# Kernel optimization log

Hardware: AMD Instinct MI355X
Metric: run time of the kernel (lower is better)

## Reference

```python
import jax, jax.numpy as jnp
import numpy as np

HIDDEN = 1024
HEADS = 16
HEAD_DIM = HIDDEN // HEADS
ROPE_THETA = 10000.0
WINDOW = 128
NEG_INF = -1e9


def _rope_cos_sin(seq_len, head_dim, theta, dtype):
    # inv_freq: [dh/2]; emb = concat([freqs, freqs]) to match rotate-half convention
    inv_freq = 1.0 / (theta ** (jnp.arange(0, head_dim, 2, dtype=jnp.float32) / head_dim))
    pos = jnp.arange(seq_len, dtype=jnp.float32)
    freqs = jnp.einsum('s,d->sd', pos, inv_freq)          # [S, dh/2]
    emb = jnp.concatenate([freqs, freqs], axis=-1)        # [S, dh]
    return jnp.cos(emb).astype(dtype), jnp.sin(emb).astype(dtype)


def _apply_rope(x, cos, sin):
    # x: [B, S, H, dh]; cos/sin: [S, dh] broadcast over batch and heads
    x1, x2 = jnp.split(x, 2, axis=-1)
    half_rot = jnp.concatenate([-x2, x1], axis=-1)
    c = cos[None, :, None, :]
    s = sin[None, :, None, :]
    return x * c + half_rot * s


def setup_inputs() -> dict:
    key = jax.random.key(0)
    k1, k2, k3, k4, k5 = jax.random.split(key, 5)
    std = 0.02
    return {
        'hidden_states': jax.random.normal(k1, (2, 2048, HIDDEN), dtype=jnp.float32),
        'Wq': jax.random.normal(k2, (HIDDEN, HEADS, HEAD_DIM), dtype=jnp.float32) * std,
        'Wk': jax.random.normal(k3, (HIDDEN, HEADS, HEAD_DIM), dtype=jnp.float32) * std,
        'Wv': jax.random.normal(k4, (HIDDEN, HEADS, HEAD_DIM), dtype=jnp.float32) * std,
        'Wo': jax.random.normal(k5, (HEADS, HEAD_DIM, HIDDEN), dtype=jnp.float32) * std,
    }


def reference(hidden_states, Wq, Wk, Wv, Wo):
    B, S, D = hidden_states.shape
    x4 = hidden_states.reshape(B, S, HEADS, HEAD_DIM)
    cos, sin = _rope_cos_sin(S, HEAD_DIM, ROPE_THETA, hidden_states.dtype)
    # RoPE applied to raw hidden states (pre-projection), per original module
    q_in = _apply_rope(x4, cos, sin).reshape(B, S, D)
    k_in = q_in  # query and key get identical RoPE of the same tensor
    v_in = hidden_states

    q = jnp.einsum('bsd,dhk->bshk', q_in, Wq)  # [B,S,H,dh]
    k = jnp.einsum('bsd,dhk->bshk', k_in, Wk)
    v = jnp.einsum('bsd,dhk->bshk', v_in, Wv)

    scale = 1.0 / jnp.sqrt(jnp.asarray(HEAD_DIM, dtype=q.dtype))
    scores = jnp.einsum('bqhd,bkhd->bhqk', q, k) * scale  # [B,H,S,S]

    # sliding-window mask: |i - j| < WINDOW
    pos = jnp.arange(S)
    win = jnp.abs(pos[:, None] - pos[None, :]) < WINDOW   # [S,S] bool
    scores = jnp.where(win[None, None, :, :], scores, NEG_INF)

    probs = jax.nn.softmax(scores, axis=-1)
    out = jnp.einsum('bhqk,bkhd->bqhd', probs, v)          # [B,S,H,dh]
    return jnp.einsum('bqhd,hdo->bqo', out, Wo)            # [B,S,D]
```

## Files before the change

### kernel.cpp

```cpp
#include <hip/hip_runtime.h>
#include <hip/hip_bf16.h>
#include <cstdint>
#include <cmath>

typedef __bf16 bf16_t;
typedef __bf16 bf16x8 __attribute__((ext_vector_type(8)));
typedef __bf16 bf16x4 __attribute__((ext_vector_type(4)));
typedef float  f32x4  __attribute__((ext_vector_type(4)));

#define MFMA16(a, b, c) __builtin_amdgcn_mfma_f32_16x16x32_bf16(a, b, c, 0, 0, 0)

constexpr int   SS    = 2048;
constexpr int   DD    = 1024;
constexpr int   HH    = 16;
constexpr float SCALE = 0.125f;
constexpr float L2E   = 1.44269504088896f;

__device__ __forceinline__ bool detect_fp32(const uint16_t* w) {
    uint16_t v = w[threadIdx.x & 63];
    int e = (v >> 7) & 0xFF;
    unsigned long long m = __ballot(e >= 0x80);
    return __popcll(m) >= 4;
}

__device__ __forceinline__ float ldin(const void* p, size_t i, bool f32) {
    return f32 ? ((const float*)p)[i] : (float)((const bf16_t*)p)[i];
}

__device__ __forceinline__ void gload_lds16(const bf16_t* g, bf16_t* l) {
    __builtin_amdgcn_global_load_lds(
        (const __attribute__((address_space(1))) void*)(g),
        (__attribute__((address_space(3))) void*)(l), 16, 0, 0);
}

__global__ __launch_bounds__(256) void prep_kernel(
    const void* __restrict__ hidden, const void* __restrict__ Wq,
    const void* __restrict__ Wk, const void* __restrict__ Wv,
    const void* __restrict__ Wo,
    bf16_t* __restrict__ roped, bf16_t* __restrict__ hiddenb,
    bf16_t* __restrict__ WqT, bf16_t* __restrict__ WkT,
    bf16_t* __restrict__ WvT, bf16_t* __restrict__ WoT) {
    const bool f32 = detect_fp32((const uint16_t*)Wq);
    __shared__ bf16_t tile[32][33];
    if (blockIdx.x < 1024) {
        int gid = blockIdx.x * 256 + threadIdx.x;
        int ic = (gid & 3) * 8;
        int h  = (gid >> 2) & 15;
        int s  = (gid >> 6) & 2047;
        int b  = gid >> 17;
        size_t base = ((size_t)(b * SS + s)) * DD + h * 64 + ic;
        float x[8], y[8];
        if (f32) {
            const float* hp = (const float*)hidden;
            f32x4 x0 = *(const f32x4*)(hp + base);
            f32x4 x1 = *(const f32x4*)(hp + base + 4);
            f32x4 y0 = *(const f32x4*)(hp + base + 32);
            f32x4 y1 = *(const f32x4*)(hp + base + 36);
#pragma unroll
            for (int j = 0; j < 4; ++j) {
                x[j] = x0[j]; x[4 + j] = x1[j];
                y[j] = y0[j]; y[4 + j] = y1[j];
            }
        } else {
            const bf16_t* hp = (const bf16_t*)hidden;
            bf16x8 xv = *(const bf16x8*)(hp + base);
            bf16x8 yv = *(const bf16x8*)(hp + base + 32);
#pragma unroll
            for (int j = 0; j < 8; ++j) { x[j] = (float)xv[j]; y[j] = (float)yv[j]; }
        }
        bf16x8 ro, rh;
#pragma unroll
        for (int j = 0; j < 8; ++j) {
            int i = ic + j;
            float invf = exp2f(-(float)i * (13.287712379549449f / 32.0f));
            float sn, cs;
            __sincosf((float)s * invf, &sn, &cs);
            ro[j]  = (bf16_t)(x[j] * cs - y[j] * sn);
            rh[j]  = (bf16_t)(y[j] * cs + x[j] * sn);
        }
        *(bf16x8*)(roped + base)      = ro;
        *(bf16x8*)(roped + base + 32) = rh;
        if (f32) {
            bf16x8 hb0, hb1;
#pragma unroll
            for (int j = 0; j < 8; ++j) { hb0[j] = (bf16_t)x[j]; hb1[j] = (bf16_t)y[j]; }
            *(bf16x8*)(hiddenb + base)      = hb0;
            *(bf16x8*)(hiddenb + base + 32) = hb1;
        }
    } else {
        int w = blockIdx.x - 1024;
        int z = w >> 10;
        int yy = (w >> 5) & 31, xx = w & 31;
        const void* src = (z == 0) ? Wq : (z == 1) ? Wk : (z == 2) ? Wv : Wo;
        bf16_t*     dst = (z == 0) ? WqT : (z == 1) ? WkT : (z == 2) ? WvT : WoT;
        int tx = threadIdx.x & 31, ty = threadIdx.x >> 5;
        int x0 = xx * 32, y0 = yy * 32;
#pragma unroll
        for (int j = 0; j < 4; ++j)
            tile[ty + j * 8][tx] =
                (bf16_t)ldin(src, (size_t)(y0 + ty + j * 8) * DD + x0 + tx, f32);
        __syncthreads();
#pragma unroll
        for (int j = 0; j < 4; ++j)
            dst[(size_t)(x0 + ty + j * 8) * DD + y0 + tx] = tile[tx][ty + j * 8];
    }
}

__device__ __forceinline__ void stage_a128(const bf16_t* A, int m0, int k0,
                                           bf16_t* As, int tid) {
#pragma unroll
    for (int i = 0; i < 4; ++i) {
        int c = tid + i * 256;
        int r = c >> 3, g = (c & 7) ^ (r & 7);
        gload_lds16(A + (size_t)(m0 + r) * DD + k0 + g * 8, As + c * 8);
    }
}
__device__ __forceinline__ void stage_b64(const bf16_t* Bt, int n0, int k0,
                                          bf16_t* Bs, int tid) {
#pragma unroll
    for (int i = 0; i < 2; ++i) {
        int c = tid + i * 256;
        int r = c >> 3, g = (c & 7) ^ (r & 7);
        gload_lds16(Bt + (size_t)(n0 + r) * DD + k0 + g * 8, Bs + c * 8);
    }
}

__global__ __launch_bounds__(256, 3) void gemm_qkv(
    const bf16_t* __restrict__ roped, const void* __restrict__ hidden_raw,
    const bf16_t* __restrict__ hiddenb, const uint16_t* __restrict__ wdet,
    const bf16_t* __restrict__ WqT, const bf16_t* __restrict__ WkT,
    const bf16_t* __restrict__ WvT,
    bf16_t* __restrict__ Qo, bf16_t* __restrict__ Ko, bf16_t* __restrict__ Vt) {
    __shared__ __align__(16) bf16_t As[128 * 64];
    __shared__ __align__(16) bf16_t Bs[128 * 64];
    const int tid = threadIdx.x, lane = tid & 63, quad = lane >> 4, l16 = lane & 15;
    const int wave = tid >> 6, wm = (wave >> 1) * 64, wn = (wave & 1) * 64;
    const int sw = l16 & 7;

    const int lin = blockIdx.x;
    const int xcd = lin & 7;
    const int t8  = lin >> 3;
    const int z   = t8 >> 5;
    const int mb  = t8 & 31;
    const int m0  = mb * 128, n0 = xcd * 128;

    const bf16_t* A;
    const bf16_t* B;
    if (z == 0)      { A = roped; B = WqT; }
    else if (z == 1) { A = roped; B = WkT; }
    else {
        const bool f32 = detect_fp32(wdet);
        A = f32 ? hiddenb : (const bf16_t*)hidden_raw;
        B = WvT;
    }

    f32x4 acc[4][4];
#pragma unroll
    for (int i = 0; i < 4; ++i)
#pragma unroll
        for (int j = 0; j < 4; ++j) acc[i][j] = (f32x4)0.0f;

    for (int k0 = 0; k0 < DD; k0 += 64) {
        stage_a128(A, m0, k0, As, tid);
        stage_a128(B, n0, k0, Bs, tid);
        __syncthreads();
#pragma unroll
        for (int half = 0; half < 2; ++half) {
            const int h4 = half * 4;
            bf16x8 af[4], bf[4];
#pragma unroll
            for (int t = 0; t < 4; ++t) {
                af[t] = *(const bf16x8*)(As + (wm + t * 16 + l16) * 64 + ((h4 + quad) ^ sw) * 8);
                bf[t] = *(const bf16x8*)(Bs + (wn + t * 16 + l16) * 64 + ((h4 + quad) ^ sw) * 8);
            }
#pragma unroll
            for (int i = 0; i < 4; ++i)
#pragma unroll
                for (int j = 0; j < 4; ++j)
                    acc[i][j] = MFMA16(af[i], bf[j], acc[i][j]);
        }
        __syncthreads();
    }

    if (z < 2) {
        bf16_t* O = (z == 0) ? Qo : Ko;
#pragma unroll
        for (int i = 0; i < 4; ++i) {
            int mbase = m0 + wm + i * 16 + quad * 4;
            int b = mbase >> 11, sl = mbase & 2047;
#pragma unroll
            for (int j = 0; j < 4; ++j) {
                int n = n0 + wn + j * 16 + l16;
                int h = n >> 6, d = n & 63;
                size_t base = (((size_t)b * HH + h) * SS + sl) * 64 + d;
#pragma unroll
                for (int r = 0; r < 4; ++r)
                    O[base + 64 * r] = (bf16_t)acc[i][j][r];
            }
        }
    } else {
#pragma unroll
        for (int i = 0; i < 4; ++i) {
            int mbase = m0 + wm + i * 16 + quad * 4;
            int b = mbase >> 11, sl = mbase & 2047;
#pragma unroll
            for (int j = 0; j < 4; ++j) {
                int n = n0 + wn + j * 16 + l16;
                int h = n >> 6, d = n & 63;
                bf16x4 v;
                v[0] = (bf16_t)acc[i][j][0]; v[1] = (bf16_t)acc[i][j][1];
                v[2] = (bf16_t)acc[i][j][2]; v[3] = (bf16_t)acc[i][j][3];
                *(bf16x4*)(Vt + (((size_t)b * HH + h) * 64 + d) * SS + sl) = v;
            }
        }
    }
}

__global__ __launch_bounds__(256) void attn_kernel(
    const bf16_t* __restrict__ Q, const bf16_t* __restrict__ Kk,
    const bf16_t* __restrict__ Vt, bf16_t* __restrict__ attn) {
    __shared__ __align__(16) bf16_t Ks[2][32 * 64];
    __shared__ __align__(16) bf16_t Vs[2][64 * 32];
    __shared__ __align__(16) bf16_t Pl[4][16 * 40];
    const int tid = threadIdx.x, wave = tid >> 6, lane = tid & 63;
    const int quad = lane >> 4, l16 = lane & 15;
    const int sw7 = l16 & 7, sw3 = l16 & 3;

    int lin = (blockIdx.x >> 3) + 128 * (blockIdx.x & 7);
    const int qb0 = (lin & 31) * 64;
    const int h   = (lin >> 5) & 15;
    const int b   = lin >> 9;
    const int qw  = qb0 + wave * 16;

    const size_t bh = (size_t)b * HH + h;
    const bf16_t* Qp = Q  + bh * SS * 64;
    const bf16_t* Kp = Kk + bh * SS * 64;
    const bf16_t* Vp = Vt + bh * 64 * SS;
    bf16_t* P = &Pl[wave][0];

    bf16x8 q0 = *(const bf16x8*)(Qp + (size_t)(qw + l16) * 64 + quad * 8);
    bf16x8 q1 = *(const bf16x8*)(Qp + (size_t)(qw + l16) * 64 + 32 + quad * 8);

    f32x4 Oacc[4];
#pragma unroll
    for (int t = 0; t < 4; ++t) Oacc[t] = (f32x4)0.0f;
    float lsum[4] = {0.f, 0.f, 0.f, 0.f};

    int lo = qb0 - 127; if (lo < 0) lo = 0; lo &= ~31;
    int hi = qb0 + 63 + 127; if (hi > SS - 1) hi = SS - 1;

    const int krow = tid >> 3, kcol = ((tid & 7) ^ (krow & 7)) * 8;
    const int vrow = tid >> 2, vcol = ((tid & 3) ^ (vrow & 3)) * 8;

    int parity = 0;
    for (int kt = lo; kt <= hi; kt += 32, parity ^= 1) {
        gload_lds16(Kp + (size_t)(kt + krow) * 64 + kcol, &Ks[parity][0] + tid * 8);
        gload_lds16(Vp + (size_t)vrow * SS + kt + vcol, &Vs[parity][0] + tid * 8);
        __syncthreads();

        const bf16_t* Kl = &Ks[parity][0];
        const bf16_t* Vl = &Vs[parity][0];
        bf16x8 k00 = *(const bf16x8*)(Kl + l16 * 64 + (quad ^ sw7) * 8);
        bf16x8 k01 = *(const bf16x8*)(Kl + l16 * 64 + ((quad + 4) ^ sw7) * 8);
        bf16x8 k10 = *(const bf16x8*)(Kl + (16 + l16) * 64 + (quad ^ sw7) * 8);
        bf16x8 k11 = *(const bf16x8*)(Kl + (16 + l16) * 64 + ((quad + 4) ^ sw7) * 8);
        bf16x8 vf[4];
#pragma unroll
        for (int t = 0; t < 4; ++t)
            vf[t] = *(const bf16x8*)(Vl + (t * 16 + l16) * 32 + (quad ^ sw3) * 8);

        __builtin_amdgcn_s_setprio(1);
        f32x4 s0 = MFMA16(q0, k00, (f32x4)0.0f);  s0 = MFMA16(q1, k01, s0);
        f32x4 s1 = MFMA16(q0, k10, (f32x4)0.0f);  s1 = MFMA16(q1, k11, s1);
        __builtin_amdgcn_s_setprio(0);

        const int kr0 = kt + l16, kr1 = kt + 16 + l16;
#pragma unroll
        for (int r = 0; r < 4; ++r) {
            int qa = qw + quad * 4 + r;
            int d0 = qa - kr0; if (d0 < 0) d0 = -d0;
            int d1 = qa - kr1; if (d1 < 0) d1 = -d1;
            float p0 = (d0 < 128) ? exp2f(s0[r] * (SCALE * L2E)) : 0.0f;
            float p1 = (d1 < 128) ? exp2f(s1[r] * (SCALE * L2E)) : 0.0f;
            lsum[r] += p0 + p1;
            P[(quad * 4 + r) * 40 + l16]      = (bf16_t)p0;
            P[(quad * 4 + r) * 40 + 16 + l16] = (bf16_t)p1;
        }
        __asm__ volatile("s_waitcnt lgkmcnt(0)" ::: "memory");
        bf16x8 pf = *(const bf16x8*)(P + l16 * 40 + quad * 8);
        __builtin_amdgcn_s_setprio(1);
#pragma unroll
        for (int t = 0; t < 4; ++t)
            Oacc[t] = MFMA16(pf, vf[t], Oacc[t]);
        __builtin_amdgcn_s_setprio(0);
    }

#pragma unroll
    for (int r = 0; r < 4; ++r) {
        float l = lsum[r];
        l += __shfl_xor(l, 1, 64);
        l += __shfl_xor(l, 2, 64);
        l += __shfl_xor(l, 4, 64);
        l += __shfl_xor(l, 8, 64);
        float inv = 1.0f / l;
        int sa = qw + quad * 4 + r;
        size_t base = (((size_t)b * SS + sa) * HH + h) * 64 + l16;
        attn[base]      = (bf16_t)(Oacc[0][r] * inv);
        attn[base + 16] = (bf16_t)(Oacc[1][r] * inv);
        attn[base + 32] = (bf16_t)(Oacc[2][r] * inv);
        attn[base + 48] = (bf16_t)(Oacc[3][r] * inv);
    }
}

__global__ __launch_bounds__(256, 4) void gemm_out_kernel(
    const bf16_t* __restrict__ A, const bf16_t* __restrict__ WoT,
    const uint16_t* __restrict__ wdet, void* __restrict__ out) {
    __shared__ __align__(16) bf16_t As[128 * 64];
    __shared__ __align__(16) bf16_t B1[64 * 64];
    const int tid = threadIdx.x, lane = tid & 63, quad = lane >> 4, l16 = lane & 15;
    const int wave = tid >> 6, wm = (wave >> 1) * 64, wn = (wave & 1) * 32;
    const int sw = l16 & 7;

    const int lin = blockIdx.x;
    const int xcd = lin & 7, s = lin >> 3;
    const int mb = (xcd >> 1) * 8 + (s >> 3);
    const int nb = (xcd & 1) * 8 + (s & 7);
    const int m0 = mb * 128, n0 = nb * 64;

    f32x4 acc[4][2];
#pragma unroll
    for (int i = 0; i < 4; ++i)
#pragma unroll
        for (int j = 0; j < 2; ++j) acc[i][j] = (f32x4)0.0f;

    for (int k0 = 0; k0 < DD; k0 += 64) {
        stage_a128(A, m0, k0, As, tid);
        stage_b64(WoT, n0, k0, B1, tid);
        __syncthreads();
#pragma unroll
        for (int half = 0; half < 2; ++half) {
            const int h4 = half * 4;
            bf16x8 af[4], b1f[2];
#pragma unroll
            for (int t = 0; t < 4; ++t)
                af[t] = *(const bf16x8*)(As + (wm + t * 16 + l16) * 64 + ((h4 + quad) ^ sw) * 8);
#pragma unroll
            for (int t = 0; t < 2; ++t)
                b1f[t] = *(const bf16x8*)(B1 + (wn + t * 16 + l16) * 64 + ((h4 + quad) ^ sw) * 8);
#pragma unroll
            for (int i = 0; i < 4; ++i)
#pragma unroll
                for (int j = 0; j < 2; ++j)
                    acc[i][j] = MFMA16(af[i], b1f[j], acc[i][j]);
        }
        __syncthreads();
    }

    const bool f32 = detect_fp32(wdet);
#pragma unroll
    for (int i = 0; i < 4; ++i) {
        int mbase = m0 + wm + i * 16 + quad * 4;
#pragma unroll
        for (int j = 0; j < 2; ++j) {
            int n = n0 + wn + j * 16 + l16;
#pragma unroll
            for (int r = 0; r < 4; ++r) {
                size_t idx = (size_t)(mbase + r) * DD + n;
                if (f32) ((float*)out)[idx] = acc[i][j][r];
                else     ((bf16_t*)out)[idx] = (bf16_t)acc[i][j][r];
            }
        }
    }
}

extern "C" void kernel_launch(void* const* d_in, const int* in_sizes, int n_in,
                              void* d_out, int out_size, void* d_ws, size_t ws_size,
                              hipStream_t stream) {
    const void* hidden = d_in[0];
    const void* Wq = d_in[1];
    const void* Wk = d_in[2];
    const void* Wv = d_in[3];
    const void* Wo = d_in[4];
    const uint16_t* wdet = (const uint16_t*)d_in[1];
    char* ws = (char*)d_ws;

    bf16_t* roped   = (bf16_t*)(ws);
    bf16_t* hiddenb = (bf16_t*)(ws + ( 8u << 20));
    bf16_t* WqT     = (bf16_t*)(ws + (16u << 20));
    bf16_t* WkT     = (bf16_t*)(ws + (18u << 20));
    bf16_t* WvT     = (bf16_t*)(ws + (20u << 20));
    bf16_t* WoT     = (bf16_t*)(ws + (22u << 20));
    bf16_t* Qb      = (bf16_t*)(ws + (24u << 20));
    bf16_t* Kb      = (bf16_t*)(ws + (32u << 20));
    bf16_t* Vt      = (bf16_t*)(ws + (40u << 20));
    bf16_t* attn    = roped;

    hipLaunchKernelGGL(prep_kernel, dim3(5120), dim3(256), 0, stream,
                       hidden, Wq, Wk, Wv, Wo, roped, hiddenb,
                       WqT, WkT, WvT, WoT);
    hipLaunchKernelGGL(gemm_qkv, dim3(768), dim3(256), 0, stream,
                       roped, hidden, hiddenb, wdet, WqT, WkT, WvT, Qb, Kb, Vt);
    hipLaunchKernelGGL(attn_kernel, dim3(1024), dim3(256), 0, stream,
                       Qb, Kb, Vt, attn);
    hipLaunchKernelGGL(gemm_out_kernel, dim3(512), dim3(256), 0, stream,
                       attn, WoT, wdet, d_out);
}
```

Baseline: 157.8 us.

## Use 32x32 MFMA in GEMMs and widen attention tiles to 128 queries

Both GEMM kernels switch from 16x16x32 to 32x32x16 bf16 MFMA with 16-wide accumulators, which changes the fragment loads and the epilogue index mapping. The goal is fewer LDS reads per MFMA. The attention kernel now uses 512-thread blocks covering 128 queries, with 64-key K/V tiles. Half the threads load K and half load V, so each block issues fewer barriers and loads per key. The trade-off is higher register and LDS pressure, and attention runs with half as many blocks.

```diff
diff --git a/kernel.cpp b/kernel.cpp
--- a/kernel.cpp
+++ b/kernel.cpp
@@ -7,8 +7,10 @@
 typedef __bf16 bf16x8 __attribute__((ext_vector_type(8)));
 typedef __bf16 bf16x4 __attribute__((ext_vector_type(4)));
 typedef float  f32x4  __attribute__((ext_vector_type(4)));
+typedef float  f32x16 __attribute__((ext_vector_type(16)));
 
 #define MFMA16(a, b, c) __builtin_amdgcn_mfma_f32_16x16x32_bf16(a, b, c, 0, 0, 0)
+#define MFMA32(a, b, c) __builtin_amdgcn_mfma_f32_32x32x16_bf16(a, b, c, 0, 0, 0)
 
 constexpr int   SS    = 2048;
 constexpr int   DD    = 1024;
@@ -133,9 +135,10 @@
     bf16_t* __restrict__ Qo, bf16_t* __restrict__ Ko, bf16_t* __restrict__ Vt) {
     __shared__ __align__(16) bf16_t As[128 * 64];
     __shared__ __align__(16) bf16_t Bs[128 * 64];
-    const int tid = threadIdx.x, lane = tid & 63, quad = lane >> 4, l16 = lane & 15;
+    const int tid = threadIdx.x, lane = tid & 63;
+    const int l32 = lane & 31, kh = lane >> 5;
     const int wave = tid >> 6, wm = (wave >> 1) * 64, wn = (wave & 1) * 64;
-    const int sw = l16 & 7;
+    const int sw = l32 & 7;
 
     const int lin = blockIdx.x;
     const int xcd = lin & 7;
@@ -154,30 +157,27 @@
         B = WvT;
     }
 
-    f32x4 acc[4][4];
-#pragma unroll
-    for (int i = 0; i < 4; ++i)
-#pragma unroll
-        for (int j = 0; j < 4; ++j) acc[i][j] = (f32x4)0.0f;
+    f32x16 acc[2][2];
+#pragma unroll
+    for (int i = 0; i < 2; ++i)
+#pragma unroll
+        for (int j = 0; j < 2; ++j) acc[i][j] = (f32x16)0.0f;
 
     for (int k0 = 0; k0 < DD; k0 += 64) {
         stage_a128(A, m0, k0, As, tid);
         stage_a128(B, n0, k0, Bs, tid);
         __syncthreads();
 #pragma unroll
-        for (int half = 0; half < 2; ++half) {
-            const int h4 = half * 4;
-            bf16x8 af[4], bf[4];
-#pragma unroll
-            for (int t = 0; t < 4; ++t) {
-                af[t] = *(const bf16x8*)(As + (wm + t * 16 + l16) * 64 + ((h4 + quad) ^ sw) * 8);
-                bf[t] = *(const bf16x8*)(Bs + (wn + t * 16 + l16) * 64 + ((h4 + quad) ^ sw) * 8);
-            }
-#pragma unroll
-            for (int i = 0; i < 4; ++i)
-#pragma unroll
-                for (int j = 0; j < 4; ++j)
-                    acc[i][j] = MFMA16(af[i], bf[j], acc[i][j]);
+        for (int kk = 0; kk < 4; ++kk) {
+            const int c8 = (kk * 2 + kh) ^ sw;
+            bf16x8 a0 = *(const bf16x8*)(As + (wm      + l32) * 64 + c8 * 8);
+            bf16x8 a1 = *(const bf16x8*)(As + (wm + 32 + l32) * 64 + c8 * 8);
+            bf16x8 b0 = *(const bf16x8*)(Bs + (wn      + l32) * 64 + c8 * 8);
+            bf16x8 b1 = *(const bf16x8*)(Bs + (wn + 32 + l32) * 64 + c8 * 8);
+            acc[0][0] = MFMA32(a0, b0, acc[0][0]);
+            acc[0][1] = MFMA32(a0, b1, acc[0][1]);
+            acc[1][0] = MFMA32(a1, b0, acc[1][0]);
+            acc[1][1] = MFMA32(a1, b1, acc[1][1]);
         }
         __syncthreads();
     }
@@ -185,51 +185,59 @@
     if (z < 2) {
         bf16_t* O = (z == 0) ? Qo : Ko;
 #pragma unroll
-        for (int i = 0; i < 4; ++i) {
-            int mbase = m0 + wm + i * 16 + quad * 4;
-            int b = mbase >> 11, sl = mbase & 2047;
-#pragma unroll
-            for (int j = 0; j < 4; ++j) {
-                int n = n0 + wn + j * 16 + l16;
-                int h = n >> 6, d = n & 63;
-                size_t base = (((size_t)b * HH + h) * SS + sl) * 64 + d;
-#pragma unroll
-                for (int r = 0; r < 4; ++r)
-                    O[base + 64 * r] = (bf16_t)acc[i][j][r];
+        for (int i = 0; i < 2; ++i) {
+#pragma unroll
+            for (int j = 0; j < 2; ++j) {
+                int n = n0 + wn + j * 32 + l32;
+                int hh = n >> 6, d = n & 63;
+#pragma unroll
+                for (int q4 = 0; q4 < 4; ++q4) {
+                    int row = m0 + wm + i * 32 + q4 * 8 + kh * 4;
+                    int bb = row >> 11, sl = row & 2047;
+                    size_t base = (((size_t)bb * HH + hh) * SS + sl) * 64 + d;
+#pragma unroll
+                    for (int r = 0; r < 4; ++r)
+                        O[base + 64 * r] = (bf16_t)acc[i][j][q4 * 4 + r];
+                }
             }
         }
     } else {
 #pragma unroll
-        for (int i = 0; i < 4; ++i) {
-            int mbase = m0 + wm + i * 16 + quad * 4;
-            int b = mbase >> 11, sl = mbase & 2047;
-#pragma unroll
-            for (int j = 0; j < 4; ++j) {
-                int n = n0 + wn + j * 16 + l16;
-                int h = n >> 6, d = n & 63;
-                bf16x4 v;
-                v[0] = (bf16_t)acc[i][j][0]; v[1] = (bf16_t)acc[i][j][1];
-                v[2] = (bf16_t)acc[i][j][2]; v[3] = (bf16_t)acc[i][j][3];
-                *(bf16x4*)(Vt + (((size_t)b * HH + h) * 64 + d) * SS + sl) = v;
+        for (int i = 0; i < 2; ++i) {
+#pragma unroll
+            for (int j = 0; j < 2; ++j) {
+                int n = n0 + wn + j * 32 + l32;
+                int hh = n >> 6, d = n & 63;
+#pragma unroll
+                for (int q4 = 0; q4 < 4; ++q4) {
+                    int row = m0 + wm + i * 32 + q4 * 8 + kh * 4;
+                    int bb = row >> 11, sl = row & 2047;
+                    bf16x4 v;
+                    v[0] = (bf16_t)acc[i][j][q4 * 4 + 0];
+                    v[1] = (bf16_t)acc[i][j][q4 * 4 + 1];
+                    v[2] = (bf16_t)acc[i][j][q4 * 4 + 2];
+                    v[3] = (bf16_t)acc[i][j][q4 * 4 + 3];
+                    *(bf16x4*)(Vt + (((size_t)bb * HH + hh) * 64 + d) * SS + sl) = v;
+                }
             }
         }
     }
 }
 
-__global__ __launch_bounds__(256) void attn_kernel(
+__global__ __launch_bounds__(512) void attn_kernel(
     const bf16_t* __restrict__ Q, const bf16_t* __restrict__ Kk,
     const bf16_t* __restrict__ Vt, bf16_t* __restrict__ attn) {
-    __shared__ __align__(16) bf16_t Ks[2][32 * 64];
-    __shared__ __align__(16) bf16_t Vs[2][64 * 32];
-    __shared__ __align__(16) bf16_t Pl[4][16 * 40];
+    __shared__ __align__(16) bf16_t Ks[2][64 * 64];
+    __shared__ __align__(16) bf16_t Vs[2][64 * 64];
+    __shared__ __align__(16) bf16_t Pl[8][16 * 72];
     const int tid = threadIdx.x, wave = tid >> 6, lane = tid & 63;
     const int quad = lane >> 4, l16 = lane & 15;
-    const int sw7 = l16 & 7, sw3 = l16 & 3;
-
-    int lin = (blockIdx.x >> 3) + 128 * (blockIdx.x & 7);
-    const int qb0 = (lin & 31) * 64;
-    const int h   = (lin >> 5) & 15;
-    const int b   = lin >> 9;
+    const int sw7 = l16 & 7;
+
+    int lin = (blockIdx.x >> 3) + 64 * (blockIdx.x & 7);
+    const int qb0 = (lin & 15) * 128;
+    const int h   = (lin >> 4) & 15;
+    const int b   = lin >> 8;
     const int qw  = qb0 + wave * 16;
 
     const size_t bh = (size_t)b * HH + h;
@@ -246,52 +254,60 @@
     for (int t = 0; t < 4; ++t) Oacc[t] = (f32x4)0.0f;
     float lsum[4] = {0.f, 0.f, 0.f, 0.f};
 
-    int lo = qb0 - 127; if (lo < 0) lo = 0; lo &= ~31;
-    int hi = qb0 + 63 + 127; if (hi > SS - 1) hi = SS - 1;
-
-    const int krow = tid >> 3, kcol = ((tid & 7) ^ (krow & 7)) * 8;
-    const int vrow = tid >> 2, vcol = ((tid & 3) ^ (vrow & 3)) * 8;
+    int lo = qb0 - 127; if (lo < 0) lo = 0; lo &= ~63;
+    int hi = qb0 + 127 + 127; if (hi > SS - 1) hi = SS - 1;
 
     int parity = 0;
-    for (int kt = lo; kt <= hi; kt += 32, parity ^= 1) {
-        gload_lds16(Kp + (size_t)(kt + krow) * 64 + kcol, &Ks[parity][0] + tid * 8);
-        gload_lds16(Vp + (size_t)vrow * SS + kt + vcol, &Vs[parity][0] + tid * 8);
+    for (int kt = lo; kt <= hi; kt += 64, parity ^= 1) {
+#pragma unroll
+        for (int i = 0; i < 2; ++i) {
+            int c = (tid & 255) + i * 256;
+            int r = c >> 3, g = ((c & 7) ^ (r & 7)) * 8;
+            if (tid < 256)
+                gload_lds16(Kp + (size_t)(kt + r) * 64 + g, &Ks[parity][0] + c * 8);
+            else
+                gload_lds16(Vp + (size_t)r * SS + kt + g, &Vs[parity][0] + c * 8);
+        }
         __syncthreads();
 
         const bf16_t* Kl = &Ks[parity][0];
         const bf16_t* Vl = &Vs[parity][0];
-        bf16x8 k00 = *(const bf16x8*)(Kl + l16 * 64 + (quad ^ sw7) * 8);
-        bf16x8 k01 = *(const bf16x8*)(Kl + l16 * 64 + ((quad + 4) ^ sw7) * 8);
-        bf16x8 k10 = *(const bf16x8*)(Kl + (16 + l16) * 64 + (quad ^ sw7) * 8);
-        bf16x8 k11 = *(const bf16x8*)(Kl + (16 + l16) * 64 + ((quad + 4) ^ sw7) * 8);
-        bf16x8 vf[4];
-#pragma unroll
-        for (int t = 0; t < 4; ++t)
-            vf[t] = *(const bf16x8*)(Vl + (t * 16 + l16) * 32 + (quad ^ sw3) * 8);
-
+
+        f32x4 s[4];
         __builtin_amdgcn_s_setprio(1);
-        f32x4 s0 = MFMA16(q0, k00, (f32x4)0.0f);  s0 = MFMA16(q1, k01, s0);
-        f32x4 s1 = MFMA16(q0, k10, (f32x4)0.0f);  s1 = MFMA16(q1, k11, s1);
+#pragma unroll
+        for (int ks = 0; ks < 4; ++ks) {
+            bf16x8 ka = *(const bf16x8*)(Kl + (ks * 16 + l16) * 64 + ((quad    ) ^ sw7) * 8);
+            bf16x8 kb = *(const bf16x8*)(Kl + (ks * 16 + l16) * 64 + ((quad + 4) ^ sw7) * 8);
+            s[ks] = MFMA16(q0, ka, (f32x4)0.0f);
+            s[ks] = MFMA16(q1, kb, s[ks]);
+        }
         __builtin_amdgcn_s_setprio(0);
 
-        const int kr0 = kt + l16, kr1 = kt + 16 + l16;
-#pragma unroll
-        for (int r = 0; r < 4; ++r) {
-            int qa = qw + quad * 4 + r;
-            int d0 = qa - kr0; if (d0 < 0) d0 = -d0;
-            int d1 = qa - kr1; if (d1 < 0) d1 = -d1;
-            float p0 = (d0 < 128) ? exp2f(s0[r] * (SCALE * L2E)) : 0.0f;
-            float p1 = (d1 < 128) ? exp2f(s1[r] * (SCALE * L2E)) : 0.0f;
-            lsum[r] += p0 + p1;
-            P[(quad * 4 + r) * 40 + l16]      = (bf16_t)p0;
-            P[(quad * 4 + r) * 40 + 16 + l16] = (bf16_t)p1;
+#pragma unroll
+        for (int ks = 0; ks < 4; ++ks) {
+            const int kr = kt + ks * 16 + l16;
+#pragma unroll
+            for (int r = 0; r < 4; ++r) {
+                int qa = qw + quad * 4 + r;
+                int dd = qa - kr; if (dd < 0) dd = -dd;
+                float p = (dd < 128) ? exp2f(s[ks][r] * (SCALE * L2E)) : 0.0f;
+                lsum[r] += p;
+                P[(quad * 4 + r) * 72 + ks * 16 + l16] = (bf16_t)p;
+            }
         }
         __asm__ volatile("s_waitcnt lgkmcnt(0)" ::: "memory");
-        bf16x8 pf = *(const bf16x8*)(P + l16 * 40 + quad * 8);
+        __builtin_amdgcn_sched_barrier(0);
+        bf16x8 pf0 = *(const bf16x8*)(P + l16 * 72 + quad * 8);
+        bf16x8 pf1 = *(const bf16x8*)(P + l16 * 72 + 32 + quad * 8);
         __builtin_amdgcn_s_setprio(1);
 #pragma unroll
-        for (int t = 0; t < 4; ++t)
-            Oacc[t] = MFMA16(pf, vf[t], Oacc[t]);
+        for (int t = 0; t < 4; ++t) {
+            bf16x8 v0 = *(const bf16x8*)(Vl + (t * 16 + l16) * 64 + ((quad    ) ^ sw7) * 8);
+            bf16x8 v1 = *(const bf16x8*)(Vl + (t * 16 + l16) * 64 + ((quad + 4) ^ sw7) * 8);
+            Oacc[t] = MFMA16(pf0, v0, Oacc[t]);
+            Oacc[t] = MFMA16(pf1, v1, Oacc[t]);
+        }
         __builtin_amdgcn_s_setprio(0);
     }
 
@@ -317,9 +333,10 @@
     const uint16_t* __restrict__ wdet, void* __restrict__ out) {
     __shared__ __align__(16) bf16_t As[128 * 64];
     __shared__ __align__(16) bf16_t B1[64 * 64];
-    const int tid = threadIdx.x, lane = tid & 63, quad = lane >> 4, l16 = lane & 15;
+    const int tid = threadIdx.x, lane = tid & 63;
+    const int l32 = lane & 31, kh = lane >> 5;
     const int wave = tid >> 6, wm = (wave >> 1) * 64, wn = (wave & 1) * 32;
-    const int sw = l16 & 7;
+    const int sw = l32 & 7;
 
     const int lin = blockIdx.x;
     const int xcd = lin & 7, s = lin >> 3;
@@ -327,47 +344,37 @@
     const int nb = (xcd & 1) * 8 + (s & 7);
     const int m0 = mb * 128, n0 = nb * 64;
 
-    f32x4 acc[4][2];
-#pragma unroll
-    for (int i = 0; i < 4; ++i)
-#pragma unroll
-        for (int j = 0; j < 2; ++j) acc[i][j] = (f32x4)0.0f;
+    f32x16 acc[2];
+    acc[0] = (f32x16)0.0f; acc[1] = (f32x16)0.0f;
 
     for (int k0 = 0; k0 < DD; k0 += 64) {
         stage_a128(A, m0, k0, As, tid);
         stage_b64(WoT, n0, k0, B1, tid);
         __syncthreads();
 #pragma unroll
-        for (int half = 0; half < 2; ++half) {
-            const int h4 = half * 4;
-            bf16x8 af[4], b1f[2];
-#pragma unroll
-            for (int t = 0; t < 4; ++t)
-                af[t] = *(const bf16x8*)(As + (wm + t * 16 + l16) * 64 + ((h4 + quad) ^ sw) * 8);
-#pragma unroll
-            for (int t = 0; t < 2; ++t)
-                b1f[t] = *(const bf16x8*)(B1 + (wn + t * 16 + l16) * 64 + ((h4 + quad) ^ sw) * 8);
-#pragma unroll
-            for (int i = 0; i < 4; ++i)
-#pragma unroll
-                for (int j = 0; j < 2; ++j)
-                    acc[i][j] = MFMA16(af[i], b1f[j], acc[i][j]);
+        for (int kk = 0; kk < 4; ++kk) {
+            const int c8 = (kk * 2 + kh) ^ sw;
+            bf16x8 a0 = *(const bf16x8*)(As + (wm      + l32) * 64 + c8 * 8);
+            bf16x8 a1 = *(const bf16x8*)(As + (wm + 32 + l32) * 64 + c8 * 8);
+            bf16x8 b0 = *(const bf16x8*)(B1 + (wn      + l32) * 64 + c8 * 8);
+            acc[0] = MFMA32(a0, b0, acc[0]);
+            acc[1] = MFMA32(a1, b0, acc[1]);
         }
         __syncthreads();
     }
 
     const bool f32 = detect_fp32(wdet);
-#pragma unroll
-    for (int i = 0; i < 4; ++i) {
-        int mbase = m0 + wm + i * 16 + quad * 4;
-#pragma unroll
-        for (int j = 0; j < 2; ++j) {
-            int n = n0 + wn + j * 16 + l16;
+    const int n = n0 + wn + l32;
+#pragma unroll
+    for (int i = 0; i < 2; ++i) {
+#pragma unroll
+        for (int q4 = 0; q4 < 4; ++q4) {
+            int row = m0 + wm + i * 32 + q4 * 8 + kh * 4;
 #pragma unroll
             for (int r = 0; r < 4; ++r) {
-                size_t idx = (size_t)(mbase + r) * DD + n;
-                if (f32) ((float*)out)[idx] = acc[i][j][r];
-                else     ((bf16_t*)out)[idx] = (bf16_t)acc[i][j][r];
+                size_t idx = (size_t)(row + r) * DD + n;
+                if (f32) ((float*)out)[idx] = acc[i][q4 * 4 + r];
+                else     ((bf16_t*)out)[idx] = (bf16_t)acc[i][q4 * 4 + r];
             }
         }
     }
@@ -400,7 +407,7 @@
                        WqT, WkT, WvT, WoT);
     hipLaunchKernelGGL(gemm_qkv, dim3(768), dim3(256), 0, stream,
                        roped, hidden, hiddenb, wdet, WqT, WkT, WvT, Qb, Kb, Vt);
-    hipLaunchKernelGGL(attn_kernel, dim3(1024), dim3(256), 0, stream,
+    hipLaunchKernelGGL(attn_kernel, dim3(512), dim3(512), 0, stream,
                        Qb, Kb, Vt, attn);
     hipLaunchKernelGGL(gemm_out_kernel, dim3(512), dim3(256), 0, stream,
                        attn, WoT, wdet, d_out);
```

Result: no change. 158.8 us (+0.7%).
